# Performance work log

Hardware: AMD Instinct MI355X
Metric: run time of the kernel (lower is better)

Reference implementation:

```python
import jax, jax.numpy as jnp
import numpy as np

NODE_IN = 163   # sum of X_MAP category sizes
HIDDEN = 64
N_NODES = 100_000
N_EDGES = 1_600_000
N_GRAPHS = 1024
SLOPE = 0.01    # F.leaky_relu default negative slope


def _linear_init(key, fan_in, fan_out):
    kw, kb = jax.random.split(key)
    bound = 1.0 / np.sqrt(fan_in)
    W = jax.random.uniform(kw, (fan_in, fan_out), jnp.float32, -bound, bound)
    b = jax.random.uniform(kb, (fan_out,), jnp.float32, -bound, bound)
    return W, b


def setup_inputs() -> dict:
    key = jax.random.key(0)
    ks = jax.random.split(key, 8)
    x = jax.random.normal(ks[0], (N_NODES, NODE_IN), jnp.float32)
    edge_index = jax.random.randint(ks[1], (2, N_EDGES), 0, N_NODES)
    batch = jnp.sort(jax.random.randint(ks[2], (N_NODES,), 0, N_GRAPHS))
    W0, b0 = _linear_init(ks[3], NODE_IN, HIDDEN)
    W1, b1 = _linear_init(ks[4], HIDDEN, HIDDEN)
    W2, b2 = _linear_init(ks[5], HIDDEN, HIDDEN)
    fc1_W, fc1_b = _linear_init(ks[6], HIDDEN, HIDDEN)
    fc2_W, fc2_b = _linear_init(ks[7], HIDDEN, 1)
    return {"x": x, "edge_index": edge_index, "batch": batch,
            "W0": W0, "b0": b0, "W1": W1, "b1": b1, "W2": W2, "b2": b2,
            "fc1_W": fc1_W, "fc1_b": fc1_b, "fc2_W": fc2_W, "fc2_b": fc2_b}


def reference(x, edge_index, batch, W0, b0, W1, b1, W2, b2, fc1_W, fc1_b, fc2_W, fc2_b):
    src, dst = edge_index[0], edge_index[1]
    # GCN symmetric norm with self-loops: deg[i] = 1 + in-degree(i)
    deg = jax.ops.segment_sum(jnp.ones(N_EDGES, x.dtype), dst, N_NODES) + 1.0
    dis = jax.lax.rsqrt(deg)               # deg^{-1/2}
    edge_norm = dis[src] * dis[dst]        # [E]
    self_norm = dis * dis                  # deg^{-1} for self-loop term

    def gcn_conv(h, W, b):
        h = h @ W                                   # [N, hidden]
        msg = h[src] * edge_norm[:, None]           # gather + scale, [E, hidden]
        agg = jax.ops.segment_sum(msg, dst, N_NODES)
        agg = agg + h * self_norm[:, None]          # self-loop contribution
        return agg + b

    h = x
    for W, b in ((W0, b0), (W1, b1), (W2, b2)):
        h = jax.nn.leaky_relu(gcn_conv(h, W, b), SLOPE)
        # dropout: eval mode (identity)

    # global_mean_pool over batch segments
    counts = jax.ops.segment_sum(jnp.ones(N_NODES, h.dtype), batch, N_GRAPHS)
    pooled = jax.ops.segment_sum(h, batch, N_GRAPHS) / jnp.maximum(counts, 1.0)[:, None]

    out = jax.nn.leaky_relu(pooled @ fc1_W + fc1_b, SLOPE)
    return (out @ fc2_W + fc2_b).squeeze(-1)       # [N_GRAPHS]
```

## Files before the change

kernel.cpp:

```cpp
#include <hip/hip_runtime.h>

#define NN 100000
#define NE 1600000
#define NG 1024
#define NODE_IN 163
#define SLOPE 0.01f
#define NBUK 391
#define BUKSH 8
#define EPB 8192
#define NBLK ((NE + EPB - 1) / EPB)

typedef short s16x8 __attribute__((ext_vector_type(8)));
typedef float f32x4 __attribute__((ext_vector_type(4)));

__device__ __forceinline__ unsigned short bf16_rne(float x) {
  unsigned u = __float_as_uint(x);
  return (unsigned short)((u + 0x7FFFu + ((u >> 16) & 1u)) >> 16);
}
__device__ __forceinline__ float bf16_f32(unsigned short h) {
  return __uint_as_float(((unsigned)h) << 16);
}

__global__ void k_hist(const int* __restrict__ dst, int* __restrict__ bh, int E) {
  __shared__ int h[NBUK];
  for (int i = threadIdx.x; i < NBUK; i += 256) h[i] = 0;
  __syncthreads();
  int beg = blockIdx.x * EPB, end = min(E, beg + EPB);
  for (int e = beg + threadIdx.x; e < end; e += 256) atomicAdd(&h[dst[e] >> BUKSH], 1);
  __syncthreads();
  for (int i = threadIdx.x; i < NBUK; i += 256) bh[blockIdx.x * NBUK + i] = h[i];
}

__global__ void k_bucket_scan(int* __restrict__ bh, int* __restrict__ btot) {
  __shared__ int s[256];
  int bucket = blockIdx.x, tid = threadIdx.x;
  int v = (tid < NBLK) ? bh[tid * NBUK + bucket] : 0;
  s[tid] = v;
  __syncthreads();
  for (int off = 1; off < 256; off <<= 1) {
    int t = (tid >= off) ? s[tid - off] : 0;
    __syncthreads();
    s[tid] += t;
    __syncthreads();
  }
  if (tid < NBLK) bh[tid * NBUK + bucket] = s[tid] - v;
  if (tid == 255) btot[bucket] = s[255];
}

__global__ void k_btot_scan(const int* __restrict__ btot, int* __restrict__ boffs, int E) {
  __shared__ int s[512];
  int tid = threadIdx.x;
  int v = (tid < NBUK) ? btot[tid] : 0;
  s[tid] = v;
  __syncthreads();
  for (int off = 1; off < 512; off <<= 1) {
    int t = (tid >= off) ? s[tid - off] : 0;
    __syncthreads();
    s[tid] += t;
    __syncthreads();
  }
  if (tid < NBUK) boffs[tid] = s[tid] - v;
  if (tid == 0) boffs[NBUK] = E;
}

__global__ void k_scatter(const int* __restrict__ src, const int* __restrict__ dst,
                          const int* __restrict__ bh, const int* __restrict__ boffs,
                          unsigned* __restrict__ bedge, int E) {
  __shared__ int cur[NBUK];
  for (int i = threadIdx.x; i < NBUK; i += 256)
    cur[i] = boffs[i] + bh[blockIdx.x * NBUK + i];
  __syncthreads();
  int beg = blockIdx.x * EPB, end = min(E, beg + EPB);
  for (int e = beg + threadIdx.x; e < end; e += 256) {
    int d = dst[e];
    int pos = atomicAdd(&cur[d >> BUKSH], 1);
    bedge[pos] = (unsigned)src[e] | ((unsigned)(d & 255) << 17);
  }
}

__global__ void k_b2csr(const unsigned* __restrict__ bedge, const int* __restrict__ boffs,
                        int* __restrict__ offs, float* __restrict__ dis,
                        int* __restrict__ csr, int N) {
  __shared__ int lcnt[256];
  __shared__ int s[256];
  __shared__ int lcur[256];
  int b = blockIdx.x, tid = threadIdx.x;
  int beg = boffs[b], end = boffs[b + 1];
  lcnt[tid] = 0;
  __syncthreads();
  for (int e = beg + tid; e < end; e += 256) atomicAdd(&lcnt[bedge[e] >> 17], 1);
  __syncthreads();
  int v = lcnt[tid];
  s[tid] = v;
  __syncthreads();
  for (int off = 1; off < 256; off <<= 1) {
    int t = (tid >= off) ? s[tid - off] : 0;
    __syncthreads();
    s[tid] += t;
    __syncthreads();
  }
  int o = s[tid] - v;
  int node = (b << BUKSH) + tid;
  if (node <= N) offs[node] = beg + o;
  if (node < N) dis[node] = rsqrtf((float)(v + 1));
  lcur[tid] = o;
  __syncthreads();
  for (int e = beg + tid; e < end; e += 256) {
    unsigned w = bedge[e];
    int p = atomicAdd(&lcur[w >> 17], 1);
    csr[beg + p] = (int)(w & 0x1FFFFu);
  }
}

__global__ void k_wsplit(const float* __restrict__ W, short* __restrict__ hi,
                         short* __restrict__ lo, int K, int KP) {
  int idx = blockIdx.x * 256 + threadIdx.x;
  if (idx >= 64 * KP) return;
  int c = idx / KP, kk = idx - c * KP;
  float v = (kk < K) ? W[(size_t)kk * 64 + c] : 0.f;
  unsigned short h = bf16_rne(v);
  hi[idx] = (short)h;
  lo[idx] = (short)bf16_rne(v - bf16_f32(h));
}

template<int K, int KP>
__launch_bounds__(256)
__global__ void k_gemm(const float* __restrict__ X, const short* __restrict__ Whi,
                       const short* __restrict__ Wlo, const float* __restrict__ disv,
                       unsigned short* __restrict__ Y, int N) {
  constexpr int KC = KP / 32;
  constexpr int PA = 40;
  constexpr int PB = 40;
  __shared__ __align__(16) short sAh[2][128 * PA];
  __shared__ __align__(16) short sAl[2][128 * PA];
  __shared__ __align__(16) short sBh[2][64 * PB];
  __shared__ __align__(16) short sBl[2][64 * PB];

  const int tid = threadIdx.x;
  const int lane = tid & 63, wv = tid >> 6;
  const int l15 = lane & 15, l4 = lane >> 4;
  const int gbase = blockIdx.x << 7;

  const int arow = tid >> 1, akh = (tid & 1) << 4;
  int grow = gbase + arow;
  if (K != KP) grow = min(grow, N - 1);
  const float* xr = X + (size_t)grow * K;
  const int bcol = tid >> 2, bk8 = (tid & 3) << 3;

  float4 ra0, ra1, ra2, ra3;
  s16x8 rbh, rbl;

  auto loadA = [&](int c) {
    if (K != KP && c == KC - 1) {
      ra0 = ra1 = ra2 = ra3 = make_float4(0.f, 0.f, 0.f, 0.f);
      if (akh == 0) { ra0.x = xr[160]; ra0.y = xr[161]; ra0.z = xr[162]; }
    } else {
      const float* p = xr + c * 32 + akh;
      ra0 = *(const float4*)(p);
      ra1 = *(const float4*)(p + 4);
      ra2 = *(const float4*)(p + 8);
      ra3 = *(const float4*)(p + 12);
    }
  };
  auto loadB = [&](int c) {
    const size_t o = (size_t)bcol * KP + c * 32 + bk8;
    rbh = *(const s16x8*)(Whi + o);
    rbl = *(const s16x8*)(Wlo + o);
  };
  auto writeLDS = [&](int b) {
    short hb[16], lb[16];
    float v[16] = {ra0.x, ra0.y, ra0.z, ra0.w, ra1.x, ra1.y, ra1.z, ra1.w,
                   ra2.x, ra2.y, ra2.z, ra2.w, ra3.x, ra3.y, ra3.z, ra3.w};
    #pragma unroll
    for (int j = 0; j < 16; ++j) {
      unsigned short h = bf16_rne(v[j]);
      hb[j] = (short)h;
      lb[j] = (short)bf16_rne(v[j] - bf16_f32(h));
    }
    short* ah = sAh[b] + arow * PA + akh;
    *(s16x8*)(ah) = *(const s16x8*)(hb);
    *(s16x8*)(ah + 8) = *(const s16x8*)(hb + 8);
    short* al = sAl[b] + arow * PA + akh;
    *(s16x8*)(al) = *(const s16x8*)(lb);
    *(s16x8*)(al + 8) = *(const s16x8*)(lb + 8);
    *(s16x8*)(sBh[b] + bcol * PB + bk8) = rbh;
    *(s16x8*)(sBl[b] + bcol * PB + bk8) = rbl;
  };

  f32x4 acc[2][4];
  #pragma unroll
  for (int rt = 0; rt < 2; ++rt)
    #pragma unroll
    for (int ct = 0; ct < 4; ++ct) acc[rt][ct] = (f32x4){0.f, 0.f, 0.f, 0.f};

  loadA(0); loadB(0); writeLDS(0);
  __syncthreads();

  #pragma unroll 1
  for (int c = 0; c < KC; ++c) {
    if (c + 1 < KC) { loadA(c + 1); loadB(c + 1); }
    const int b = c & 1;
    const int aoff0 = (wv * 32 + l15) * PA + l4 * 8;
    const int aoff1 = aoff0 + 16 * PA;
    s16x8 a0h = *(const s16x8*)(sAh[b] + aoff0);
    s16x8 a0l = *(const s16x8*)(sAl[b] + aoff0);
    s16x8 a1h = *(const s16x8*)(sAh[b] + aoff1);
    s16x8 a1l = *(const s16x8*)(sAl[b] + aoff1);
    #pragma unroll
    for (int ct = 0; ct < 4; ++ct) {
      const int boff = (ct * 16 + l15) * PB + l4 * 8;
      s16x8 bh = *(const s16x8*)(sBh[b] + boff);
      s16x8 bl = *(const s16x8*)(sBl[b] + boff);
      acc[0][ct] = __builtin_amdgcn_mfma_f32_16x16x32_bf16(a0h, bh, acc[0][ct], 0, 0, 0);
      acc[0][ct] = __builtin_amdgcn_mfma_f32_16x16x32_bf16(a0l, bh, acc[0][ct], 0, 0, 0);
      acc[0][ct] = __builtin_amdgcn_mfma_f32_16x16x32_bf16(a0h, bl, acc[0][ct], 0, 0, 0);
      acc[1][ct] = __builtin_amdgcn_mfma_f32_16x16x32_bf16(a1h, bh, acc[1][ct], 0, 0, 0);
      acc[1][ct] = __builtin_amdgcn_mfma_f32_16x16x32_bf16(a1l, bh, acc[1][ct], 0, 0, 0);
      acc[1][ct] = __builtin_amdgcn_mfma_f32_16x16x32_bf16(a1h, bl, acc[1][ct], 0, 0, 0);
    }
    if (c + 1 < KC) { writeLDS((c + 1) & 1); __syncthreads(); }
  }

  const int rb = gbase + wv * 32;
  #pragma unroll
  for (int rt = 0; rt < 2; ++rt) {
    #pragma unroll
    for (int j = 0; j < 4; ++j) {
      int row = rb + rt * 16 + l4 * 4 + j;
      if (row < N) {
        float d = disv[row];
        unsigned short* yp = Y + ((size_t)row << 6) + l15;
        yp[0]  = bf16_rne(acc[rt][0][j] * d);
        yp[16] = bf16_rne(acc[rt][1][j] * d);
        yp[32] = bf16_rne(acc[rt][2][j] * d);
        yp[48] = bf16_rne(acc[rt][3][j] * d);
      }
    }
  }
}

__launch_bounds__(256)
__global__ void k_agg(const unsigned short* __restrict__ G, const int* __restrict__ offs,
                      const int* __restrict__ csr, const float* __restrict__ dis,
                      const float* __restrict__ bias, float* __restrict__ H, int N) {
  int node = blockIdx.x * 4 + (threadIdx.x >> 6);
  if (node >= N) return;
  int lane = threadIdx.x & 63;
  const unsigned short* Gl = G + lane;
  int beg = offs[node], end = offs[node + 1];
  float acc = bf16_f32(Gl[(size_t)node << 6]);
  int e = beg;
  for (; e + 16 <= end; e += 16) {
    int s[16];
    #pragma unroll
    for (int j = 0; j < 16; ++j) s[j] = csr[e + j];
    #pragma unroll
    for (int j = 0; j < 16; ++j) acc += bf16_f32(Gl[(size_t)s[j] << 6]);
  }
  for (; e + 4 <= end; e += 4) {
    int s0 = csr[e], s1 = csr[e + 1], s2 = csr[e + 2], s3 = csr[e + 3];
    acc += bf16_f32(Gl[(size_t)s0 << 6]);
    acc += bf16_f32(Gl[(size_t)s1 << 6]);
    acc += bf16_f32(Gl[(size_t)s2 << 6]);
    acc += bf16_f32(Gl[(size_t)s3 << 6]);
  }
  for (; e < end; ++e) acc += bf16_f32(Gl[(size_t)csr[e] << 6]);
  acc = acc * dis[node] + bias[lane];
  H[((size_t)node << 6) + lane] = (acc > 0.f) ? acc : SLOPE * acc;
}

__launch_bounds__(64)
__global__ void k_pool(const float* __restrict__ H, const int* __restrict__ batch,
                       const float* __restrict__ f1W, const float* __restrict__ f1b,
                       const float* __restrict__ f2W, const float* __restrict__ f2b,
                       float* __restrict__ out, int N) {
  int g = blockIdx.x;
  int lane = threadIdx.x;
  int lo = 0, hi = N;
  while (lo < hi) { int m = (lo + hi) >> 1; if (batch[m] < g) lo = m + 1; else hi = m; }
  int beg = lo;
  hi = N;
  while (lo < hi) { int m = (lo + hi) >> 1; if (batch[m] < g + 1) lo = m + 1; else hi = m; }
  int end = lo;
  float acc = 0.f;
  for (int r = beg; r < end; ++r) acc += H[(size_t)r * 64 + lane];
  float c = (float)(end - beg);
  acc /= (c < 1.f ? 1.f : c);
  __shared__ float p[64];
  p[lane] = acc;
  __syncthreads();
  float q = f1b[lane];
  #pragma unroll
  for (int k = 0; k < 64; ++k) q += p[k] * f1W[k * 64 + lane];
  q = (q > 0.f) ? q : SLOPE * q;
  float v = q * f2W[lane];
  #pragma unroll
  for (int off = 32; off > 0; off >>= 1) v += __shfl_down(v, off, 64);
  if (lane == 0) out[g] = v + f2b[0];
}

extern "C" void kernel_launch(void* const* d_in, const int* in_sizes, int n_in,
                              void* d_out, int out_size, void* d_ws, size_t ws_size,
                              hipStream_t stream) {
  const float* x    = (const float*)d_in[0];
  const int*  eidx  = (const int*)d_in[1];
  const int*  batch = (const int*)d_in[2];
  const float* W0 = (const float*)d_in[3];
  const float* b0 = (const float*)d_in[4];
  const float* W1 = (const float*)d_in[5];
  const float* b1 = (const float*)d_in[6];
  const float* W2 = (const float*)d_in[7];
  const float* b2 = (const float*)d_in[8];
  const float* f1W = (const float*)d_in[9];
  const float* f1b = (const float*)d_in[10];
  const float* f2W = (const float*)d_in[11];
  const float* f2b = (const float*)d_in[12];
  float* out = (float*)d_out;

  const int N = NN, E = NE;
  const int* src  = eidx;
  const int* dstp = eidx + E;

  const size_t NPAD = 100096;
  char* w = (char*)d_ws;
  float* H     = (float*)w; w += NPAD * 64 * 4;
  unsigned short* G = (unsigned short*)w; w += NPAD * 64 * 2;
  int*   csr   = (int*)w;   w += (size_t)E * 4;
  int*   offs  = (int*)w;   w += (size_t)(N + 4) * 4;
  float* dis   = (float*)w; w += (size_t)N * 4;
  int*   bh    = (int*)w;   w += (size_t)NBLK * NBUK * 4;
  int*   btot  = (int*)w;   w += (NBUK + 1) * 4;
  int*   boffs = (int*)w;   w += (NBUK + 4) * 4;
  short* wt0h  = (short*)w; w += 64 * 192 * 2;
  short* wt0l  = (short*)w; w += 64 * 192 * 2;
  short* wt1h  = (short*)w; w += 64 * 64 * 2;
  short* wt1l  = (short*)w; w += 64 * 64 * 2;
  short* wt2h  = (short*)w; w += 64 * 64 * 2;
  short* wt2l  = (short*)w; w += 64 * 64 * 2;
  unsigned* bedge = (unsigned*)H;

  k_wsplit<<<48, 256, 0, stream>>>(W0, wt0h, wt0l, NODE_IN, 192);
  k_wsplit<<<16, 256, 0, stream>>>(W1, wt1h, wt1l, 64, 64);
  k_wsplit<<<16, 256, 0, stream>>>(W2, wt2h, wt2l, 64, 64);

  k_hist<<<NBLK, 256, 0, stream>>>(dstp, bh, E);
  k_bucket_scan<<<NBUK, 256, 0, stream>>>(bh, btot);
  k_btot_scan<<<1, 512, 0, stream>>>(btot, boffs, E);
  k_scatter<<<NBLK, 256, 0, stream>>>(src, dstp, bh, boffs, bedge, E);
  k_b2csr<<<NBUK, 256, 0, stream>>>(bedge, boffs, offs, dis, csr, N);

  const int NTB = (N + 127) / 128;
  k_gemm<NODE_IN, 192><<<NTB, 256, 0, stream>>>(x, wt0h, wt0l, dis, G, N);
  k_agg<<<(N + 3) / 4, 256, 0, stream>>>(G, offs, csr, dis, b0, H, N);
  k_gemm<64, 64><<<NTB, 256, 0, stream>>>(H, wt1h, wt1l, dis, G, N);
  k_agg<<<(N + 3) / 4, 256, 0, stream>>>(G, offs, csr, dis, b1, H, N);
  k_gemm<64, 64><<<NTB, 256, 0, stream>>>(H, wt2h, wt2l, dis, G, N);
  k_agg<<<(N + 3) / 4, 256, 0, stream>>>(G, offs, csr, dis, b2, H, N);
  k_pool<<<NG, 64, 0, stream>>>(H, batch, f1W, f1b, f2W, f2b, out, N);
}
```

Before: 322.9 us.

## Process two nodes per wavefront in aggregation and read GEMM weights directly

The aggregation kernel now has each wavefront handle two adjacent nodes, interleaving their neighbor gathers in batches of eight so more independent loads are in flight at once. The launch grid is halved to match. Separately, the GEMM no longer stages the bf16 hi/lo weight tiles through shared memory and loads them straight from global memory (cache-resident) per MFMA step, which removes LDS writes and traffic. The trade-offs are more global load instructions inside the GEMM inner loop, fewer wavefronts in aggregation, and some imbalance when the two nodes' degrees differ.

Result: slower. 348.0 us (+7.8%).

```diff
diff --git a/kernel.cpp b/kernel.cpp
--- a/kernel.cpp
+++ b/kernel.cpp
@@ -130,11 +130,8 @@
                        unsigned short* __restrict__ Y, int N) {
   constexpr int KC = KP / 32;
   constexpr int PA = 40;
-  constexpr int PB = 40;
   __shared__ __align__(16) short sAh[2][128 * PA];
   __shared__ __align__(16) short sAl[2][128 * PA];
-  __shared__ __align__(16) short sBh[2][64 * PB];
-  __shared__ __align__(16) short sBl[2][64 * PB];
 
   const int tid = threadIdx.x;
   const int lane = tid & 63, wv = tid >> 6;
@@ -145,10 +142,9 @@
   int grow = gbase + arow;
   if (K != KP) grow = min(grow, N - 1);
   const float* xr = X + (size_t)grow * K;
-  const int bcol = tid >> 2, bk8 = (tid & 3) << 3;
+  const int wb = l15 * KP + l4 * 8;
 
   float4 ra0, ra1, ra2, ra3;
-  s16x8 rbh, rbl;
 
   auto loadA = [&](int c) {
     if (K != KP && c == KC - 1) {
@@ -162,11 +158,6 @@
       ra3 = *(const float4*)(p + 12);
     }
   };
-  auto loadB = [&](int c) {
-    const size_t o = (size_t)bcol * KP + c * 32 + bk8;
-    rbh = *(const s16x8*)(Whi + o);
-    rbl = *(const s16x8*)(Wlo + o);
-  };
   auto writeLDS = [&](int b) {
     short hb[16], lb[16];
     float v[16] = {ra0.x, ra0.y, ra0.z, ra0.w, ra1.x, ra1.y, ra1.z, ra1.w,
@@ -183,8 +174,6 @@
     short* al = sAl[b] + arow * PA + akh;
     *(s16x8*)(al) = *(const s16x8*)(lb);
     *(s16x8*)(al + 8) = *(const s16x8*)(lb + 8);
-    *(s16x8*)(sBh[b] + bcol * PB + bk8) = rbh;
-    *(s16x8*)(sBl[b] + bcol * PB + bk8) = rbl;
   };
 
   f32x4 acc[2][4];
@@ -193,12 +182,12 @@
     #pragma unroll
     for (int ct = 0; ct < 4; ++ct) acc[rt][ct] = (f32x4){0.f, 0.f, 0.f, 0.f};
 
-  loadA(0); loadB(0); writeLDS(0);
+  loadA(0); writeLDS(0);
   __syncthreads();
 
   #pragma unroll 1
   for (int c = 0; c < KC; ++c) {
-    if (c + 1 < KC) { loadA(c + 1); loadB(c + 1); }
+    if (c + 1 < KC) loadA(c + 1);
     const int b = c & 1;
     const int aoff0 = (wv * 32 + l15) * PA + l4 * 8;
     const int aoff1 = aoff0 + 16 * PA;
@@ -208,9 +197,9 @@
     s16x8 a1l = *(const s16x8*)(sAl[b] + aoff1);
     #pragma unroll
     for (int ct = 0; ct < 4; ++ct) {
-      const int boff = (ct * 16 + l15) * PB + l4 * 8;
-      s16x8 bh = *(const s16x8*)(sBh[b] + boff);
-      s16x8 bl = *(const s16x8*)(sBl[b] + boff);
+      const size_t bo = (size_t)(ct * 16) * KP + c * 32 + wb;
+      s16x8 bh = *(const s16x8*)(Whi + bo);
+      s16x8 bl = *(const s16x8*)(Wlo + bo);
       acc[0][ct] = __builtin_amdgcn_mfma_f32_16x16x32_bf16(a0h, bh, acc[0][ct], 0, 0, 0);
       acc[0][ct] = __builtin_amdgcn_mfma_f32_16x16x32_bf16(a0l, bh, acc[0][ct], 0, 0, 0);
       acc[0][ct] = __builtin_amdgcn_mfma_f32_16x16x32_bf16(a0h, bl, acc[0][ct], 0, 0, 0);
@@ -243,30 +232,60 @@
 __global__ void k_agg(const unsigned short* __restrict__ G, const int* __restrict__ offs,
                       const int* __restrict__ csr, const float* __restrict__ dis,
                       const float* __restrict__ bias, float* __restrict__ H, int N) {
-  int node = blockIdx.x * 4 + (threadIdx.x >> 6);
-  if (node >= N) return;
-  int lane = threadIdx.x & 63;
+  const int lane = threadIdx.x & 63;
+  const int n0 = blockIdx.x * 8 + (threadIdx.x >> 6) * 2;
+  if (n0 >= N) return;
   const unsigned short* Gl = G + lane;
-  int beg = offs[node], end = offs[node + 1];
-  float acc = bf16_f32(Gl[(size_t)node << 6]);
-  int e = beg;
-  for (; e + 16 <= end; e += 16) {
-    int s[16];
-    #pragma unroll
-    for (int j = 0; j < 16; ++j) s[j] = csr[e + j];
-    #pragma unroll
-    for (int j = 0; j < 16; ++j) acc += bf16_f32(Gl[(size_t)s[j] << 6]);
-  }
-  for (; e + 4 <= end; e += 4) {
-    int s0 = csr[e], s1 = csr[e + 1], s2 = csr[e + 2], s3 = csr[e + 3];
-    acc += bf16_f32(Gl[(size_t)s0 << 6]);
-    acc += bf16_f32(Gl[(size_t)s1 << 6]);
-    acc += bf16_f32(Gl[(size_t)s2 << 6]);
-    acc += bf16_f32(Gl[(size_t)s3 << 6]);
-  }
-  for (; e < end; ++e) acc += bf16_f32(Gl[(size_t)csr[e] << 6]);
-  acc = acc * dis[node] + bias[lane];
-  H[((size_t)node << 6) + lane] = (acc > 0.f) ? acc : SLOPE * acc;
+  int b0 = offs[n0];
+  int m0 = offs[n0 + 1];
+  int e1 = offs[n0 + 2];
+  int b1 = m0;
+  float a0 = bf16_f32(Gl[(size_t)n0 << 6]);
+  float a1 = bf16_f32(Gl[(size_t)(n0 + 1) << 6]);
+  while (b0 + 8 <= m0 && b1 + 8 <= e1) {
+    int s0[8], s1[8];
+    #pragma unroll
+    for (int j = 0; j < 8; ++j) s0[j] = csr[b0 + j];
+    #pragma unroll
+    for (int j = 0; j < 8; ++j) s1[j] = csr[b1 + j];
+    float g0[8], g1[8];
+    #pragma unroll
+    for (int j = 0; j < 8; ++j) g0[j] = bf16_f32(Gl[(size_t)s0[j] << 6]);
+    #pragma unroll
+    for (int j = 0; j < 8; ++j) g1[j] = bf16_f32(Gl[(size_t)s1[j] << 6]);
+    #pragma unroll
+    for (int j = 0; j < 8; ++j) a0 += g0[j];
+    #pragma unroll
+    for (int j = 0; j < 8; ++j) a1 += g1[j];
+    b0 += 8; b1 += 8;
+  }
+  for (; b0 + 8 <= m0; b0 += 8) {
+    int s[8];
+    #pragma unroll
+    for (int j = 0; j < 8; ++j) s[j] = csr[b0 + j];
+    float g[8];
+    #pragma unroll
+    for (int j = 0; j < 8; ++j) g[j] = bf16_f32(Gl[(size_t)s[j] << 6]);
+    #pragma unroll
+    for (int j = 0; j < 8; ++j) a0 += g[j];
+  }
+  for (; b0 < m0; ++b0) a0 += bf16_f32(Gl[(size_t)csr[b0] << 6]);
+  for (; b1 + 8 <= e1; b1 += 8) {
+    int s[8];
+    #pragma unroll
+    for (int j = 0; j < 8; ++j) s[j] = csr[b1 + j];
+    float g[8];
+    #pragma unroll
+    for (int j = 0; j < 8; ++j) g[j] = bf16_f32(Gl[(size_t)s[j] << 6]);
+    #pragma unroll
+    for (int j = 0; j < 8; ++j) a1 += g[j];
+  }
+  for (; b1 < e1; ++b1) a1 += bf16_f32(Gl[(size_t)csr[b1] << 6]);
+
+  a0 = a0 * dis[n0] + bias[lane];
+  H[((size_t)n0 << 6) + lane] = (a0 > 0.f) ? a0 : SLOPE * a0;
+  a1 = a1 * dis[n0 + 1] + bias[lane];
+  H[((size_t)(n0 + 1) << 6) + lane] = (a1 > 0.f) ? a1 : SLOPE * a1;
 }
 
 __launch_bounds__(64)
@@ -351,10 +370,10 @@
 
   const int NTB = (N + 127) / 128;
   k_gemm<NODE_IN, 192><<<NTB, 256, 0, stream>>>(x, wt0h, wt0l, dis, G, N);
-  k_agg<<<(N + 3) / 4, 256, 0, stream>>>(G, offs, csr, dis, b0, H, N);
+  k_agg<<<(N + 7) / 8, 256, 0, stream>>>(G, offs, csr, dis, b0, H, N);
   k_gemm<64, 64><<<NTB, 256, 0, stream>>>(H, wt1h, wt1l, dis, G, N);
-  k_agg<<<(N + 3) / 4, 256, 0, stream>>>(G, offs, csr, dis, b1, H, N);
+  k_agg<<<(N + 7) / 8, 256, 0, stream>>>(G, offs, csr, dis, b1, H, N);
   k_gemm<64, 64><<<NTB, 256, 0, stream>>>(H, wt2h, wt2l, dis, G, N);
-  k_agg<<<(N + 3) / 4, 256, 0, stream>>>(G, offs, csr, dis, b2, H, N);
+  k_agg<<<(N + 7) / 8, 256, 0, stream>>>(G, offs, csr, dis, b2, H, N);
   k_pool<<<NG, 64, 0, stream>>>(H, batch, f1W, f1b, f2W, f2b, out, N);
 }
```

## Split aggregation wavefront into four edge groups with vectorized bf16 gathers

Applied to the files above, without the earlier changes.

The per-node aggregation wavefront now splits its 64 lanes into 4 groups of 16. Each lane loads a ushort4 (8 bytes) of a neighbor row, so four edges are gathered at once, and the partial sums are combined with cross-lane xor shuffles. The aim is fewer, wider gather loads and more edges in flight per wavefront in the latency-bound sparse aggregation. In exchange it adds shuffle reductions and leaves only one lane group active for the final store.

After: 308.6 us. 1.05x faster.

```diff
diff --git a/kernel.cpp b/kernel.cpp
--- a/kernel.cpp
+++ b/kernel.cpp
@@ -245,28 +245,50 @@
                       const float* __restrict__ bias, float* __restrict__ H, int N) {
   int node = blockIdx.x * 4 + (threadIdx.x >> 6);
   if (node >= N) return;
-  int lane = threadIdx.x & 63;
-  const unsigned short* Gl = G + lane;
+  const int lane = threadIdx.x & 63;
+  const int g = lane >> 4, p = lane & 15;
+  const ushort4* G4 = (const ushort4*)G;
   int beg = offs[node], end = offs[node + 1];
-  float acc = bf16_f32(Gl[(size_t)node << 6]);
-  int e = beg;
-  for (; e + 16 <= end; e += 16) {
-    int s[16];
-    #pragma unroll
-    for (int j = 0; j < 16; ++j) s[j] = csr[e + j];
-    #pragma unroll
-    for (int j = 0; j < 16; ++j) acc += bf16_f32(Gl[(size_t)s[j] << 6]);
-  }
-  for (; e + 4 <= end; e += 4) {
-    int s0 = csr[e], s1 = csr[e + 1], s2 = csr[e + 2], s3 = csr[e + 3];
-    acc += bf16_f32(Gl[(size_t)s0 << 6]);
-    acc += bf16_f32(Gl[(size_t)s1 << 6]);
-    acc += bf16_f32(Gl[(size_t)s2 << 6]);
-    acc += bf16_f32(Gl[(size_t)s3 << 6]);
-  }
-  for (; e < end; ++e) acc += bf16_f32(Gl[(size_t)csr[e] << 6]);
-  acc = acc * dis[node] + bias[lane];
-  H[((size_t)node << 6) + lane] = (acc > 0.f) ? acc : SLOPE * acc;
+  float ax = 0.f, ay = 0.f, az = 0.f, aw = 0.f;
+  int e = beg + g;
+  for (; e + 12 < end; e += 16) {
+    int s0 = csr[e], s1 = csr[e + 4], s2 = csr[e + 8], s3 = csr[e + 12];
+    ushort4 v0 = G4[(size_t)s0 * 16 + p];
+    ushort4 v1 = G4[(size_t)s1 * 16 + p];
+    ushort4 v2 = G4[(size_t)s2 * 16 + p];
+    ushort4 v3 = G4[(size_t)s3 * 16 + p];
+    ax += bf16_f32(v0.x) + bf16_f32(v1.x) + bf16_f32(v2.x) + bf16_f32(v3.x);
+    ay += bf16_f32(v0.y) + bf16_f32(v1.y) + bf16_f32(v2.y) + bf16_f32(v3.y);
+    az += bf16_f32(v0.z) + bf16_f32(v1.z) + bf16_f32(v2.z) + bf16_f32(v3.z);
+    aw += bf16_f32(v0.w) + bf16_f32(v1.w) + bf16_f32(v2.w) + bf16_f32(v3.w);
+  }
+  for (; e < end; e += 4) {
+    int s = csr[e];
+    ushort4 v = G4[(size_t)s * 16 + p];
+    ax += bf16_f32(v.x); ay += bf16_f32(v.y);
+    az += bf16_f32(v.z); aw += bf16_f32(v.w);
+  }
+  #pragma unroll
+  for (int off = 16; off < 64; off <<= 1) {
+    ax += __shfl_xor(ax, off, 64);
+    ay += __shfl_xor(ay, off, 64);
+    az += __shfl_xor(az, off, 64);
+    aw += __shfl_xor(aw, off, 64);
+  }
+  if (g == 0) {
+    ushort4 sv = G4[(size_t)node * 16 + p];
+    float d = dis[node];
+    float4 bq = ((const float4*)bias)[p];
+    float ox = (ax + bf16_f32(sv.x)) * d + bq.x;
+    float oy = (ay + bf16_f32(sv.y)) * d + bq.y;
+    float oz = (az + bf16_f32(sv.z)) * d + bq.z;
+    float ow = (aw + bf16_f32(sv.w)) * d + bq.w;
+    ox = (ox > 0.f) ? ox : SLOPE * ox;
+    oy = (oy > 0.f) ? oy : SLOPE * oy;
+    oz = (oz > 0.f) ? oz : SLOPE * oz;
+    ow = (ow > 0.f) ? ow : SLOPE * ow;
+    ((float4*)(H + ((size_t)node << 6)))[p] = make_float4(ox, oy, oz, ow);
+  }
 }
 
 __launch_bounds__(64)
```
